# Kernel optimization log

Hardware: AMD Instinct MI355X
Metric: run time of the kernel (lower is better)

The kernel has to match this reference:

```python
import jax, jax.numpy as jnp
import numpy as np

B = 64          # graphs in batch
NPG = 9         # nodes per graph (max_atoms = NUM_ATOMS = 9)
N = B * NPG     # total nodes = 576
H = 128         # node_dim == hid_dim
SPEC_LEN = 1801
SPEC_COMP = 100
BOND = 3
ASL = BOND * 9 * 9  # action_space_length = 243


def _linear_init(key, fan_in, fan_out):
    # torch.nn.Linear default init: U(-1/sqrt(fan_in), 1/sqrt(fan_in)); stored as [in, out]
    kw, kb = jax.random.split(key)
    bound = 1.0 / np.sqrt(fan_in)
    W = jax.random.uniform(kw, (fan_in, fan_out), jnp.float32, -bound, bound)
    b = jax.random.uniform(kb, (fan_out,), jnp.float32, -bound, bound)
    return W, b


def setup_inputs() -> dict:
    key = jax.random.key(0)
    ks = jax.random.split(key, 10)
    node_features = jax.random.normal(ks[0], (N, H), jnp.float32)
    specs = jax.random.normal(ks[1], (B, 1, SPEC_LEN), jnp.float32)
    # len_vec[b, i] = 1 iff node i belongs to graph b (contiguous 9-node blocks)
    gid = np.repeat(np.arange(B), NPG)
    len_vec = jnp.asarray((gid[None, :] == np.arange(B)[:, None]).astype(np.float32))
    mask = jnp.zeros((B, ASL), jnp.float32)  # additive action mask (0 = allowed)
    indexmask = jax.random.randint(ks[2], (B, ASL), 0, ASL, dtype=jnp.int32)
    W1, b1 = _linear_init(ks[3], SPEC_LEN, SPEC_LEN // 2)
    W2, b2 = _linear_init(ks[4], SPEC_LEN // 2, SPEC_COMP)
    Wv1, bv1 = _linear_init(ks[5], H + SPEC_COMP, H // 2)
    Wv2, bv2 = _linear_init(ks[6], H // 2, 1)
    Wa2, ba2 = _linear_init(ks[7], 2 * H + SPEC_COMP, H)
    Wf, bf = _linear_init(ks[8], H, BOND)
    return {"node_features": node_features, "specs": specs, "len_vec": len_vec,
            "mask": mask, "indexmask": indexmask,
            "W1": W1, "b1": b1, "W2": W2, "b2": b2,
            "Wv1": Wv1, "bv1": bv1, "Wv2": Wv2, "bv2": bv2,
            "Wa2": Wa2, "ba2": ba2, "Wf": Wf, "bf": bf}


def reference(node_features, specs, len_vec, mask, indexmask,
              W1, b1, W2, b2, Wv1, bv1, Wv2, bv2, Wa2, ba2, Wf, bf):
    relu = jax.nn.relu
    n_total, hdim = node_features.shape
    bsz = specs.shape[0]
    npg = n_total // bsz

    # --- spectrum compression: [B,1801] -> [B,100] ---
    s = relu(specs[:, 0, :] @ W1 + b1)
    s = relu(s @ W2 + b2)

    # --- value head: SumPooling readout + spec -> scalar per graph ---
    readout = node_features.reshape(bsz, npg, hdim).sum(axis=1)
    v = relu(jnp.concatenate([readout, s], axis=-1) @ Wv1 + bv1) @ Wv2 + bv2  # [B,1]

    # --- pairwise action features ---
    # original: apf[i,j] = relu(cat(nf[i], nf[j], canvas[i,j])) then Linear(action_2).
    # relu is elementwise and Linear splits over the concat, so factorize:
    #   apf @ Wa2 = relu(nf)[i] @ Wa2[:H]  +  relu(nf)[j] @ Wa2[H:2H]  +  relu(canvas)[i,j] @ Wa2[2H:]
    # canvas is the block-diagonal scatter of s (s >= 0 so relu(canvas) = canvas).
    gid = jnp.arange(n_total) // npg
    same = gid[:, None] == gid[None, :]          # block-diagonal [N,N]
    nf_r = relu(node_features)
    Ai = nf_r @ Wa2[:hdim]                        # [N,H] per-row (Y2) term
    Bj = nf_r @ Wa2[hdim:2 * hdim]                # [N,H] per-col (X2) term
    D = s @ Wa2[2 * hdim:]                        # [B,H] spec-canvas term
    h = relu(Ai[:, None, :] + Bj[None, :, :]
             + jnp.where(same[:, :, None], D[gid][:, None, :], 0.0) + ba2)  # [N,N,H]

    len_matrix = (len_vec.T @ len_vec)[:, :, None]  # block-diagonal pair mask [N,N,1]
    saf = (h @ Wf + bf) * len_matrix                # [N,N,BOND]

    # --- per-graph action assembly (replaces nonzero()+pad+index_select loop) ---
    # with npg nodes per graph the nonzeros of saf are exactly the diagonal
    # npg x npg blocks, flattened (i, j, bond)-major, npg*npg*BOND == ASL.
    rows = jnp.arange(bsz)[:, None] * npg + jnp.arange(npg)[None, :]   # [B,npg]
    fp = saf[rows[:, :, None], rows[:, None, :], :].reshape(bsz, npg * npg * saf.shape[-1])
    gathered = jnp.take_along_axis(fp, indexmask.astype(jnp.int32), axis=1)
    return jax.nn.softmax(gathered + mask, axis=1), v
```

## Files before the change

### kernel.cpp

```cpp
#include <hip/hip_runtime.h>
#include <math.h>

#define BATCH 64
#define NPG 9
#define N_NODES 576
#define HD 128
#define SPEC_LEN 1801
#define S1DIM 900
#define SCOMP 100
#define ASL 243
#define NT 15
#define KC 17
#define KCH 106
#define KPAD 112

__global__ __launch_bounds__(256) void k1(const float* __restrict__ specs,
                                          const float* __restrict__ W1,
                                          const float* __restrict__ nf,
                                          const float* __restrict__ Wa2,
                                          float* __restrict__ P,
                                          float* __restrict__ AB) {
    int bb = blockIdx.x, tid = threadIdx.x;
    if (bb < NT * KC) {
        __shared__ __align__(16) float sA[KPAD * 68];
        __shared__ __align__(16) float sB[KPAD * 64];
        int nt = bb % NT, kc = bb / NT;
        int n0 = nt * 64, kb = kc * KCH;
        int klen = min(KCH, SPEC_LEN - kb);

#pragma unroll
        for (int p = 0; p < 28; ++p) {
            int e = p * 256 + tid;
            int m = e / KPAD;
            int k = e - m * KPAD;
            float v = (k < klen) ? specs[(size_t)m * SPEC_LEN + kb + k] : 0.0f;
            sA[k * 68 + m] = v;
        }
#pragma unroll
        for (int p = 0; p < 7; ++p) {
            int e = p * 256 + tid;
            int kl = e >> 4, nq = (e & 15) * 4;
            float4 v = make_float4(0.f, 0.f, 0.f, 0.f);
            if (kl < klen && (n0 + nq) < S1DIM)
                v = *(const float4*)&W1[(size_t)(kb + kl) * S1DIM + n0 + nq];
            *(float4*)&sB[kl * 64 + nq] = v;
        }
        __syncthreads();

        int tn = (tid & 15) * 4;
        int tm = (tid >> 4) * 4;
        float acc[4][4] = {};
#pragma unroll 4
        for (int k = 0; k < KPAD; ++k) {
            const float4 a = *(const float4*)&sA[k * 68 + tm];
            const float4 b = *(const float4*)&sB[k * 64 + tn];
            acc[0][0] = fmaf(a.x, b.x, acc[0][0]);
            acc[0][1] = fmaf(a.x, b.y, acc[0][1]);
            acc[0][2] = fmaf(a.x, b.z, acc[0][2]);
            acc[0][3] = fmaf(a.x, b.w, acc[0][3]);
            acc[1][0] = fmaf(a.y, b.x, acc[1][0]);
            acc[1][1] = fmaf(a.y, b.y, acc[1][1]);
            acc[1][2] = fmaf(a.y, b.z, acc[1][2]);
            acc[1][3] = fmaf(a.y, b.w, acc[1][3]);
            acc[2][0] = fmaf(a.z, b.x, acc[2][0]);
            acc[2][1] = fmaf(a.z, b.y, acc[2][1]);
            acc[2][2] = fmaf(a.z, b.z, acc[2][2]);
            acc[2][3] = fmaf(a.z, b.w, acc[2][3]);
            acc[3][0] = fmaf(a.w, b.x, acc[3][0]);
            acc[3][1] = fmaf(a.w, b.y, acc[3][1]);
            acc[3][2] = fmaf(a.w, b.z, acc[3][2]);
            acc[3][3] = fmaf(a.w, b.w, acc[3][3]);
        }

        if (n0 + tn < S1DIM) {
#pragma unroll
            for (int i = 0; i < 4; ++i) {
                float4 o = make_float4(acc[i][0], acc[i][1], acc[i][2], acc[i][3]);
                *(float4*)&P[((size_t)(kc * 64 + tm + i)) * S1DIM + n0 + tn] = o;
            }
        }
    } else {
        __shared__ float snf[4 * HD];
        int ib = (bb - NT * KC) * 4;
        snf[tid]       = fmaxf(nf[(size_t)ib * HD + tid], 0.0f);
        snf[256 + tid] = fmaxf(nf[(size_t)ib * HD + 256 + tid], 0.0f);
        __syncthreads();
        int c = tid;
        const float* __restrict__ wp = (c < HD) ? (Wa2 + c) : (Wa2 + HD * HD + (c - HD));
        float a0 = 0.f, a1 = 0.f, a2 = 0.f, a3 = 0.f;
#pragma unroll 16
        for (int k = 0; k < HD; ++k) {
            float w = wp[(size_t)k * HD];
            a0 = fmaf(snf[k], w, a0);
            a1 = fmaf(snf[HD + k], w, a1);
            a2 = fmaf(snf[2 * HD + k], w, a2);
            a3 = fmaf(snf[3 * HD + k], w, a3);
        }
        AB[(size_t)(ib + 0) * 256 + c] = a0;
        AB[(size_t)(ib + 1) * 256 + c] = a1;
        AB[(size_t)(ib + 2) * 256 + c] = a2;
        AB[(size_t)(ib + 3) * 256 + c] = a3;
    }
}

__global__ __launch_bounds__(128) void k2(const float* __restrict__ P,
                                          const float* __restrict__ b1,
                                          const float* __restrict__ W2,
                                          float* __restrict__ Pc) {
    __shared__ float sld[100];
    int m = blockIdx.x, kc9 = blockIdx.y, tid = threadIdx.x;
    int kb = kc9 * 100;
    if (tid < 100) {
        int k = kb + tid;
        float a = b1[k];
#pragma unroll
        for (int kc = 0; kc < KC; ++kc)
            a += P[((size_t)kc * 64 + m) * S1DIM + k];
        sld[tid] = fmaxf(a, 0.0f);
    }
    __syncthreads();
    if (tid < SCOMP) {
        float a = 0.0f;
#pragma unroll 10
        for (int kl = 0; kl < 100; ++kl)
            a = fmaf(sld[kl], W2[(size_t)(kb + kl) * SCOMP + tid], a);
        Pc[((size_t)kc9 * 64 + m) * SCOMP + tid] = a;
    }
}

__global__ __launch_bounds__(256) void k3(const float* __restrict__ Pc,
                                          const float* __restrict__ b2,
                                          const float* __restrict__ Wa2,
                                          const float* __restrict__ nf,
                                          const float* __restrict__ Wv1,
                                          const float* __restrict__ bv1,
                                          const float* __restrict__ Wv2,
                                          const float* __restrict__ bv2,
                                          const float* __restrict__ ba2,
                                          const float* __restrict__ Wf,
                                          const float* __restrict__ bfb,
                                          const int* __restrict__ indexmask,
                                          const float* __restrict__ mask,
                                          const float* __restrict__ AB,
                                          float* __restrict__ out,
                                          float* __restrict__ vout) {
    int m = blockIdx.x, tid = threadIdx.x;
    __shared__ __align__(16) float sAi[NPG * 132];
    __shared__ __align__(16) float sBj[NPG * 132];
    __shared__ __align__(16) float sWfT[3 * 132];
    __shared__ __align__(16) float rv[232];
    __shared__ __align__(16) float sC[HD];
    __shared__ float pD[256];
    __shared__ float pV[256];
    __shared__ float fp[ASL];
    __shared__ float red[8];

#pragma unroll
    for (int e = tid; e < NPG * 256; e += 256) {
        int i = e >> 8, c = e & 255;
        float v = AB[(size_t)(m * NPG + i) * 256 + c];
        if (c < HD) sAi[i * 132 + c] = v;
        else        sBj[i * 132 + (c - HD)] = v;
    }
    for (int e = tid; e < 3 * HD; e += 256)
        sWfT[(e % 3) * 132 + (e / 3)] = Wf[e];
    if (tid < SCOMP) {
        float a = b2[tid];
#pragma unroll
        for (int q = 0; q < 9; ++q)
            a += Pc[((size_t)q * 64 + m) * SCOMP + tid];
        rv[128 + tid] = fmaxf(a, 0.0f);
    }
    if (tid >= 128) {
        int h = tid - 128;
        float a = 0.0f;
#pragma unroll
        for (int i = 0; i < NPG; ++i) a += nf[(size_t)(m * NPG + i) * HD + h];
        rv[h] = a;
    }
    __syncthreads();

    {
        int t = tid & 127, half = tid >> 7;
        float aD = 0.0f;
#pragma unroll 10
        for (int kl = 0; kl < 50; ++kl) {
            int k = half * 50 + kl;
            aD = fmaf(rv[128 + k], Wa2[(size_t)(2 * HD + k) * HD + t], aD);
        }
        pD[tid] = aD;
        int tv = tid & 63, q = tid >> 6;
        float aV = 0.0f;
#pragma unroll 8
        for (int kl = 0; kl < 57; ++kl) {
            int k = q * 57 + kl;
            aV = fmaf(rv[k], Wv1[(size_t)k * 64 + tv], aV);
        }
        pV[tid] = aV;
    }
    __syncthreads();
    if (tid < HD) {
        sC[tid] = pD[tid] + pD[tid + 128] + ba2[tid];
    } else if (tid < 192) {
        int t = tid - 128;
        float a = fmaxf(pV[t] + pV[64 + t] + pV[128 + t] + pV[192 + t] + bv1[t], 0.0f);
        float p = a * Wv2[t];
#pragma unroll
        for (int off = 32; off; off >>= 1) p += __shfl_down(p, off, 64);
        if (tid == 128) vout[m] = p + bv2[0];
    }
    __syncthreads();

    if (tid < ASL) {
        int i = tid / 27;
        int j = (tid / 3) % 9;
        int bo = tid % 3;
        float a = bfb[bo];
        const float* pa = sAi + i * 132;
        const float* pb = sBj + j * 132;
        const float* pw = sWfT + bo * 132;
#pragma unroll 8
        for (int h = 0; h < HD; h += 4) {
            const float4 A = *(const float4*)&pa[h];
            const float4 Bv = *(const float4*)&pb[h];
            const float4 C = *(const float4*)&sC[h];
            const float4 W = *(const float4*)&pw[h];
            a = fmaf(fmaxf(A.x + Bv.x + C.x, 0.f), W.x, a);
            a = fmaf(fmaxf(A.y + Bv.y + C.y, 0.f), W.y, a);
            a = fmaf(fmaxf(A.z + Bv.z + C.z, 0.f), W.z, a);
            a = fmaf(fmaxf(A.w + Bv.w + C.w, 0.f), W.w, a);
        }
        fp[tid] = a;
    }
    __syncthreads();

    float g = -INFINITY;
    if (tid < ASL) g = fp[indexmask[(size_t)m * ASL + tid]] + mask[(size_t)m * ASL + tid];
    float mx = g;
#pragma unroll
    for (int off = 32; off; off >>= 1) mx = fmaxf(mx, __shfl_down(mx, off, 64));
    if ((tid & 63) == 0) red[tid >> 6] = mx;
    __syncthreads();
    mx = fmaxf(fmaxf(red[0], red[1]), fmaxf(red[2], red[3]));
    float e = (tid < ASL) ? __expf(g - mx) : 0.0f;
    float sm = e;
#pragma unroll
    for (int off = 32; off; off >>= 1) sm += __shfl_down(sm, off, 64);
    if ((tid & 63) == 0) red[4 + (tid >> 6)] = sm;
    __syncthreads();
    sm = red[4] + red[5] + red[6] + red[7];
    if (tid < ASL) out[(size_t)m * ASL + tid] = e / sm;
}

extern "C" void kernel_launch(void* const* d_in, const int* in_sizes, int n_in,
                              void* d_out, int out_size, void* d_ws, size_t ws_size,
                              hipStream_t stream) {
    (void)in_sizes; (void)n_in; (void)out_size; (void)ws_size;
    const float* nf    = (const float*)d_in[0];
    const float* specs = (const float*)d_in[1];
    const float* mask  = (const float*)d_in[3];
    const int*   idxm  = (const int*)d_in[4];
    const float* W1  = (const float*)d_in[5];
    const float* b1  = (const float*)d_in[6];
    const float* W2  = (const float*)d_in[7];
    const float* b2  = (const float*)d_in[8];
    const float* Wv1 = (const float*)d_in[9];
    const float* bv1 = (const float*)d_in[10];
    const float* Wv2 = (const float*)d_in[11];
    const float* bv2 = (const float*)d_in[12];
    const float* Wa2 = (const float*)d_in[13];
    const float* ba2 = (const float*)d_in[14];
    const float* Wf  = (const float*)d_in[15];
    const float* bfv = (const float*)d_in[16];
    float* out = (float*)d_out;
    float* ws  = (float*)d_ws;

    float* P  = ws;
    float* AB = P + (size_t)KC * 64 * S1DIM;
    float* Pc = AB + (size_t)N_NODES * 256;

    k1<<<dim3(NT * KC + N_NODES / 4), dim3(256), 0, stream>>>(specs, W1, nf, Wa2, P, AB);
    k2<<<dim3(BATCH, 9), dim3(128), 0, stream>>>(P, b1, W2, Pc);
    k3<<<dim3(BATCH), dim3(256), 0, stream>>>(Pc, b2, Wa2, nf,
                                              Wv1, bv1, Wv2, bv2, ba2, Wf, bfv,
                                              idxm, mask, AB, out, out + BATCH * ASL);
}
```

Baseline: 127.8 us.

## Fuse three kernels into one persistent kernel with atomic grid barriers

Merges the spectrum GEMM, its reduction/second layer, and the per-graph head into a single launch, separated by software grid barriers built on atomic counters. The K-split of the first GEMM doubles to 33 chunks of 55 so that more blocks run in the first phase. The goal is to remove two kernel launch gaps and the tail idling between stages. In exchange it adds a memset, spin-wait barrier overhead, and more partial sums to reduce. It also relies on all 639 blocks being co-resident, or the barriers will deadlock.

```diff
diff --git a/kernel.cpp b/kernel.cpp
--- a/kernel.cpp
+++ b/kernel.cpp
@@ -10,40 +10,72 @@
 #define SCOMP 100
 #define ASL 243
 #define NT 15
-#define KC 17
-#define KCH 106
-#define KPAD 112
-
-__global__ __launch_bounds__(256) void k1(const float* __restrict__ specs,
-                                          const float* __restrict__ W1,
-                                          const float* __restrict__ nf,
-                                          const float* __restrict__ Wa2,
-                                          float* __restrict__ P,
-                                          float* __restrict__ AB) {
+#define KC 33
+#define KCH 55
+#define KPAD 56
+#define G1BLK (NT * KC)
+#define GRID_BLKS (G1BLK + 144)
+
+__device__ __forceinline__ void grid_barrier(unsigned* cnt, unsigned target) {
+    __syncthreads();
+    if (threadIdx.x == 0) {
+        __threadfence();
+        atomicAdd(cnt, 1u);
+        while (atomicAdd(cnt, 0u) < target) { __builtin_amdgcn_s_sleep(8); }
+    }
+    __syncthreads();
+    __threadfence();
+}
+
+__global__ __launch_bounds__(256, 3) void kfused(
+        const float* __restrict__ specs, const float* __restrict__ W1,
+        const float* __restrict__ nf, const float* __restrict__ Wa2,
+        const float* __restrict__ b1, const float* __restrict__ W2,
+        const float* __restrict__ b2,
+        const float* __restrict__ Wv1, const float* __restrict__ bv1,
+        const float* __restrict__ Wv2, const float* __restrict__ bv2,
+        const float* __restrict__ ba2, const float* __restrict__ Wf,
+        const float* __restrict__ bfb,
+        const int* __restrict__ indexmask, const float* __restrict__ mask,
+        float* __restrict__ P, float* __restrict__ Pc, float* __restrict__ AB,
+        unsigned* __restrict__ bar,
+        float* __restrict__ out, float* __restrict__ vout) {
     int bb = blockIdx.x, tid = threadIdx.x;
-    if (bb < NT * KC) {
-        __shared__ __align__(16) float sA[KPAD * 68];
-        __shared__ __align__(16) float sB[KPAD * 64];
+
+    __shared__ union {
+        struct { float sA[KPAD * 68]; float sB[KPAD * 64]; } g1;
+        struct { float snf[4 * HD]; } ab;
+        struct { float sld[100]; } g2;
+        struct {
+            float sAi[NPG * 132]; float sBj[NPG * 132]; float sWfT[3 * 132];
+            float rv[232]; float sC[HD]; float pD[256]; float pV[256];
+            float fp[ASL]; float red[8];
+        } hd;
+    } sh;
+
+    if (bb < G1BLK) {
         int nt = bb % NT, kc = bb / NT;
         int n0 = nt * 64, kb = kc * KCH;
         int klen = min(KCH, SPEC_LEN - kb);
 
 #pragma unroll
-        for (int p = 0; p < 28; ++p) {
+        for (int p = 0; p < 14; ++p) {
             int e = p * 256 + tid;
-            int m = e / KPAD;
-            int k = e - m * KPAD;
-            float v = (k < klen) ? specs[(size_t)m * SPEC_LEN + kb + k] : 0.0f;
-            sA[k * 68 + m] = v;
-        }
-#pragma unroll
-        for (int p = 0; p < 7; ++p) {
+            int mm = e / KPAD;
+            int k = e - mm * KPAD;
+            float v = (k < klen) ? specs[(size_t)mm * SPEC_LEN + kb + k] : 0.0f;
+            sh.g1.sA[k * 68 + mm] = v;
+        }
+#pragma unroll
+        for (int p = 0; p < 4; ++p) {
             int e = p * 256 + tid;
-            int kl = e >> 4, nq = (e & 15) * 4;
-            float4 v = make_float4(0.f, 0.f, 0.f, 0.f);
-            if (kl < klen && (n0 + nq) < S1DIM)
-                v = *(const float4*)&W1[(size_t)(kb + kl) * S1DIM + n0 + nq];
-            *(float4*)&sB[kl * 64 + nq] = v;
+            if (e < 896) {
+                int kl = e >> 4, nq = (e & 15) * 4;
+                float4 v = make_float4(0.f, 0.f, 0.f, 0.f);
+                if (kl < klen && (n0 + nq) < S1DIM)
+                    v = *(const float4*)&W1[(size_t)(kb + kl) * S1DIM + n0 + nq];
+                *(float4*)&sh.g1.sB[kl * 64 + nq] = v;
+            }
         }
         __syncthreads();
 
@@ -52,8 +84,8 @@
         float acc[4][4] = {};
 #pragma unroll 4
         for (int k = 0; k < KPAD; ++k) {
-            const float4 a = *(const float4*)&sA[k * 68 + tm];
-            const float4 b = *(const float4*)&sB[k * 64 + tn];
+            const float4 a = *(const float4*)&sh.g1.sA[k * 68 + tm];
+            const float4 b = *(const float4*)&sh.g1.sB[k * 64 + tn];
             acc[0][0] = fmaf(a.x, b.x, acc[0][0]);
             acc[0][1] = fmaf(a.x, b.y, acc[0][1]);
             acc[0][2] = fmaf(a.x, b.z, acc[0][2]);
@@ -80,10 +112,9 @@
             }
         }
     } else {
-        __shared__ float snf[4 * HD];
-        int ib = (bb - NT * KC) * 4;
-        snf[tid]       = fmaxf(nf[(size_t)ib * HD + tid], 0.0f);
-        snf[256 + tid] = fmaxf(nf[(size_t)ib * HD + 256 + tid], 0.0f);
+        int ib = (bb - G1BLK) * 4;
+        sh.ab.snf[tid]       = fmaxf(nf[(size_t)ib * HD + tid], 0.0f);
+        sh.ab.snf[256 + tid] = fmaxf(nf[(size_t)ib * HD + 256 + tid], 0.0f);
         __syncthreads();
         int c = tid;
         const float* __restrict__ wp = (c < HD) ? (Wa2 + c) : (Wa2 + HD * HD + (c - HD));
@@ -91,165 +122,142 @@
 #pragma unroll 16
         for (int k = 0; k < HD; ++k) {
             float w = wp[(size_t)k * HD];
-            a0 = fmaf(snf[k], w, a0);
-            a1 = fmaf(snf[HD + k], w, a1);
-            a2 = fmaf(snf[2 * HD + k], w, a2);
-            a3 = fmaf(snf[3 * HD + k], w, a3);
+            a0 = fmaf(sh.ab.snf[k], w, a0);
+            a1 = fmaf(sh.ab.snf[HD + k], w, a1);
+            a2 = fmaf(sh.ab.snf[2 * HD + k], w, a2);
+            a3 = fmaf(sh.ab.snf[3 * HD + k], w, a3);
         }
         AB[(size_t)(ib + 0) * 256 + c] = a0;
         AB[(size_t)(ib + 1) * 256 + c] = a1;
         AB[(size_t)(ib + 2) * 256 + c] = a2;
         AB[(size_t)(ib + 3) * 256 + c] = a3;
     }
-}
-
-__global__ __launch_bounds__(128) void k2(const float* __restrict__ P,
-                                          const float* __restrict__ b1,
-                                          const float* __restrict__ W2,
-                                          float* __restrict__ Pc) {
-    __shared__ float sld[100];
-    int m = blockIdx.x, kc9 = blockIdx.y, tid = threadIdx.x;
-    int kb = kc9 * 100;
-    if (tid < 100) {
-        int k = kb + tid;
-        float a = b1[k];
-#pragma unroll
-        for (int kc = 0; kc < KC; ++kc)
-            a += P[((size_t)kc * 64 + m) * S1DIM + k];
-        sld[tid] = fmaxf(a, 0.0f);
-    }
-    __syncthreads();
-    if (tid < SCOMP) {
-        float a = 0.0f;
+
+    grid_barrier(bar + 0, GRID_BLKS);
+
+    if (bb < BATCH * 9) {
+        int m = bb & 63, q = bb >> 6;
+        int kb = q * 100;
+        if (tid < 100) {
+            int k = kb + tid;
+            float a = b1[k];
+#pragma unroll
+            for (int kc = 0; kc < KC; ++kc)
+                a += P[((size_t)kc * 64 + m) * S1DIM + k];
+            sh.g2.sld[tid] = fmaxf(a, 0.0f);
+        }
+        __syncthreads();
+        if (tid < SCOMP) {
+            float a = 0.0f;
 #pragma unroll 10
-        for (int kl = 0; kl < 100; ++kl)
-            a = fmaf(sld[kl], W2[(size_t)(kb + kl) * SCOMP + tid], a);
-        Pc[((size_t)kc9 * 64 + m) * SCOMP + tid] = a;
-    }
-}
-
-__global__ __launch_bounds__(256) void k3(const float* __restrict__ Pc,
-                                          const float* __restrict__ b2,
-                                          const float* __restrict__ Wa2,
-                                          const float* __restrict__ nf,
-                                          const float* __restrict__ Wv1,
-                                          const float* __restrict__ bv1,
-                                          const float* __restrict__ Wv2,
-                                          const float* __restrict__ bv2,
-                                          const float* __restrict__ ba2,
-                                          const float* __restrict__ Wf,
-                                          const float* __restrict__ bfb,
-                                          const int* __restrict__ indexmask,
-                                          const float* __restrict__ mask,
-                                          const float* __restrict__ AB,
-                                          float* __restrict__ out,
-                                          float* __restrict__ vout) {
-    int m = blockIdx.x, tid = threadIdx.x;
-    __shared__ __align__(16) float sAi[NPG * 132];
-    __shared__ __align__(16) float sBj[NPG * 132];
-    __shared__ __align__(16) float sWfT[3 * 132];
-    __shared__ __align__(16) float rv[232];
-    __shared__ __align__(16) float sC[HD];
-    __shared__ float pD[256];
-    __shared__ float pV[256];
-    __shared__ float fp[ASL];
-    __shared__ float red[8];
-
-#pragma unroll
-    for (int e = tid; e < NPG * 256; e += 256) {
-        int i = e >> 8, c = e & 255;
-        float v = AB[(size_t)(m * NPG + i) * 256 + c];
-        if (c < HD) sAi[i * 132 + c] = v;
-        else        sBj[i * 132 + (c - HD)] = v;
-    }
-    for (int e = tid; e < 3 * HD; e += 256)
-        sWfT[(e % 3) * 132 + (e / 3)] = Wf[e];
-    if (tid < SCOMP) {
-        float a = b2[tid];
-#pragma unroll
-        for (int q = 0; q < 9; ++q)
-            a += Pc[((size_t)q * 64 + m) * SCOMP + tid];
-        rv[128 + tid] = fmaxf(a, 0.0f);
-    }
-    if (tid >= 128) {
-        int h = tid - 128;
-        float a = 0.0f;
-#pragma unroll
-        for (int i = 0; i < NPG; ++i) a += nf[(size_t)(m * NPG + i) * HD + h];
-        rv[h] = a;
-    }
-    __syncthreads();
-
-    {
-        int t = tid & 127, half = tid >> 7;
-        float aD = 0.0f;
+            for (int kl = 0; kl < 100; ++kl)
+                a = fmaf(sh.g2.sld[kl], W2[(size_t)(kb + kl) * SCOMP + tid], a);
+            Pc[((size_t)q * 64 + m) * SCOMP + tid] = a;
+        }
+    }
+
+    grid_barrier(bar + 1, GRID_BLKS);
+
+    if (bb < BATCH) {
+        int m = bb;
+#pragma unroll
+        for (int e = tid; e < NPG * 256; e += 256) {
+            int i = e >> 8, c = e & 255;
+            float v = AB[(size_t)(m * NPG + i) * 256 + c];
+            if (c < HD) sh.hd.sAi[i * 132 + c] = v;
+            else        sh.hd.sBj[i * 132 + (c - HD)] = v;
+        }
+        for (int e = tid; e < 3 * HD; e += 256)
+            sh.hd.sWfT[(e % 3) * 132 + (e / 3)] = Wf[e];
+        if (tid < SCOMP) {
+            float a = b2[tid];
+#pragma unroll
+            for (int q = 0; q < 9; ++q)
+                a += Pc[((size_t)q * 64 + m) * SCOMP + tid];
+            sh.hd.rv[128 + tid] = fmaxf(a, 0.0f);
+        }
+        if (tid >= 128) {
+            int h = tid - 128;
+            float a = 0.0f;
+#pragma unroll
+            for (int i = 0; i < NPG; ++i) a += nf[(size_t)(m * NPG + i) * HD + h];
+            sh.hd.rv[h] = a;
+        }
+        __syncthreads();
+
+        {
+            int t = tid & 127, half = tid >> 7;
+            float aD = 0.0f;
 #pragma unroll 10
-        for (int kl = 0; kl < 50; ++kl) {
-            int k = half * 50 + kl;
-            aD = fmaf(rv[128 + k], Wa2[(size_t)(2 * HD + k) * HD + t], aD);
-        }
-        pD[tid] = aD;
-        int tv = tid & 63, q = tid >> 6;
-        float aV = 0.0f;
+            for (int kl = 0; kl < 50; ++kl) {
+                int k = half * 50 + kl;
+                aD = fmaf(sh.hd.rv[128 + k], Wa2[(size_t)(2 * HD + k) * HD + t], aD);
+            }
+            sh.hd.pD[tid] = aD;
+            int tv = tid & 63, q = tid >> 6;
+            float aV = 0.0f;
 #pragma unroll 8
-        for (int kl = 0; kl < 57; ++kl) {
-            int k = q * 57 + kl;
-            aV = fmaf(rv[k], Wv1[(size_t)k * 64 + tv], aV);
-        }
-        pV[tid] = aV;
-    }
-    __syncthreads();
-    if (tid < HD) {
-        sC[tid] = pD[tid] + pD[tid + 128] + ba2[tid];
-    } else if (tid < 192) {
-        int t = tid - 128;
-        float a = fmaxf(pV[t] + pV[64 + t] + pV[128 + t] + pV[192 + t] + bv1[t], 0.0f);
-        float p = a * Wv2[t];
-#pragma unroll
-        for (int off = 32; off; off >>= 1) p += __shfl_down(p, off, 64);
-        if (tid == 128) vout[m] = p + bv2[0];
-    }
-    __syncthreads();
-
-    if (tid < ASL) {
-        int i = tid / 27;
-        int j = (tid / 3) % 9;
-        int bo = tid % 3;
-        float a = bfb[bo];
-        const float* pa = sAi + i * 132;
-        const float* pb = sBj + j * 132;
-        const float* pw = sWfT + bo * 132;
+            for (int kl = 0; kl < 57; ++kl) {
+                int k = q * 57 + kl;
+                aV = fmaf(sh.hd.rv[k], Wv1[(size_t)k * 64 + tv], aV);
+            }
+            sh.hd.pV[tid] = aV;
+        }
+        __syncthreads();
+        if (tid < HD) {
+            sh.hd.sC[tid] = sh.hd.pD[tid] + sh.hd.pD[tid + 128] + ba2[tid];
+        } else if (tid < 192) {
+            int t = tid - 128;
+            float a = fmaxf(sh.hd.pV[t] + sh.hd.pV[64 + t] + sh.hd.pV[128 + t] +
+                            sh.hd.pV[192 + t] + bv1[t], 0.0f);
+            float p = a * Wv2[t];
+#pragma unroll
+            for (int off = 32; off; off >>= 1) p += __shfl_down(p, off, 64);
+            if (tid == 128) vout[m] = p + bv2[0];
+        }
+        __syncthreads();
+
+        if (tid < ASL) {
+            int i = tid / 27;
+            int j = (tid / 3) % 9;
+            int bo = tid % 3;
+            float a = bfb[bo];
+            const float* pa = sh.hd.sAi + i * 132;
+            const float* pb = sh.hd.sBj + j * 132;
+            const float* pw = sh.hd.sWfT + bo * 132;
 #pragma unroll 8
-        for (int h = 0; h < HD; h += 4) {
-            const float4 A = *(const float4*)&pa[h];
-            const float4 Bv = *(const float4*)&pb[h];
-            const float4 C = *(const float4*)&sC[h];
-            const float4 W = *(const float4*)&pw[h];
-            a = fmaf(fmaxf(A.x + Bv.x + C.x, 0.f), W.x, a);
-            a = fmaf(fmaxf(A.y + Bv.y + C.y, 0.f), W.y, a);
-            a = fmaf(fmaxf(A.z + Bv.z + C.z, 0.f), W.z, a);
-            a = fmaf(fmaxf(A.w + Bv.w + C.w, 0.f), W.w, a);
-        }
-        fp[tid] = a;
-    }
-    __syncthreads();
-
-    float g = -INFINITY;
-    if (tid < ASL) g = fp[indexmask[(size_t)m * ASL + tid]] + mask[(size_t)m * ASL + tid];
-    float mx = g;
-#pragma unroll
-    for (int off = 32; off; off >>= 1) mx = fmaxf(mx, __shfl_down(mx, off, 64));
-    if ((tid & 63) == 0) red[tid >> 6] = mx;
-    __syncthreads();
-    mx = fmaxf(fmaxf(red[0], red[1]), fmaxf(red[2], red[3]));
-    float e = (tid < ASL) ? __expf(g - mx) : 0.0f;
-    float sm = e;
-#pragma unroll
-    for (int off = 32; off; off >>= 1) sm += __shfl_down(sm, off, 64);
-    if ((tid & 63) == 0) red[4 + (tid >> 6)] = sm;
-    __syncthreads();
-    sm = red[4] + red[5] + red[6] + red[7];
-    if (tid < ASL) out[(size_t)m * ASL + tid] = e / sm;
+            for (int h = 0; h < HD; h += 4) {
+                const float4 A = *(const float4*)&pa[h];
+                const float4 Bv = *(const float4*)&pb[h];
+                const float4 C = *(const float4*)&sh.hd.sC[h];
+                const float4 W = *(const float4*)&pw[h];
+                a = fmaf(fmaxf(A.x + Bv.x + C.x, 0.f), W.x, a);
+                a = fmaf(fmaxf(A.y + Bv.y + C.y, 0.f), W.y, a);
+                a = fmaf(fmaxf(A.z + Bv.z + C.z, 0.f), W.z, a);
+                a = fmaf(fmaxf(A.w + Bv.w + C.w, 0.f), W.w, a);
+            }
+            sh.hd.fp[tid] = a;
+        }
+        __syncthreads();
+
+        float g = -INFINITY;
+        if (tid < ASL)
+            g = sh.hd.fp[indexmask[(size_t)m * ASL + tid]] + mask[(size_t)m * ASL + tid];
+        float mx = g;
+#pragma unroll
+        for (int off = 32; off; off >>= 1) mx = fmaxf(mx, __shfl_down(mx, off, 64));
+        if ((tid & 63) == 0) sh.hd.red[tid >> 6] = mx;
+        __syncthreads();
+        mx = fmaxf(fmaxf(sh.hd.red[0], sh.hd.red[1]), fmaxf(sh.hd.red[2], sh.hd.red[3]));
+        float e = (tid < ASL) ? __expf(g - mx) : 0.0f;
+        float sm = e;
+#pragma unroll
+        for (int off = 32; off; off >>= 1) sm += __shfl_down(sm, off, 64);
+        if ((tid & 63) == 0) sh.hd.red[4 + (tid >> 6)] = sm;
+        __syncthreads();
+        sm = sh.hd.red[4] + sh.hd.red[5] + sh.hd.red[6] + sh.hd.red[7];
+        if (tid < ASL) out[(size_t)m * ASL + tid] = e / sm;
+    }
 }
 
 extern "C" void kernel_launch(void* const* d_in, const int* in_sizes, int n_in,
@@ -272,16 +280,17 @@
     const float* ba2 = (const float*)d_in[14];
     const float* Wf  = (const float*)d_in[15];
     const float* bfv = (const float*)d_in[16];
-    float* out = (float*)d_out;
-    float* ws  = (float*)d_ws;
+    float* out  = (float*)d_out;
+    float* vout = out + BATCH * ASL;
+    float* ws   = (float*)d_ws;
 
     float* P  = ws;
     float* AB = P + (size_t)KC * 64 * S1DIM;
     float* Pc = AB + (size_t)N_NODES * 256;
-
-    k1<<<dim3(NT * KC + N_NODES / 4), dim3(256), 0, stream>>>(specs, W1, nf, Wa2, P, AB);
-    k2<<<dim3(BATCH, 9), dim3(128), 0, stream>>>(P, b1, W2, Pc);
-    k3<<<dim3(BATCH), dim3(256), 0, stream>>>(Pc, b2, Wa2, nf,
-                                              Wv1, bv1, Wv2, bv2, ba2, Wf, bfv,
-                                              idxm, mask, AB, out, out + BATCH * ASL);
+    unsigned* bar = (unsigned*)(Pc + (size_t)9 * 64 * SCOMP);
+
+    hipMemsetAsync(bar, 0, 2 * sizeof(unsigned), stream);
+    kfused<<<dim3(GRID_BLKS), dim3(256), 0, stream>>>(
+        specs, W1, nf, Wa2, b1, W2, b2, Wv1, bv1, Wv2, bv2,
+        ba2, Wf, bfv, idxm, mask, P, Pc, AB, bar, out, vout);
 }
```

New measurement: 317.3 us. 2.48x slower.
